# Performance work log

Hardware: AMD Instinct MI355X
Metric: run time of the kernel (lower is better)

The kernel has to match this reference:

```python
import jax, jax.numpy as jnp
import numpy as np

DN = ('NHWC', 'HWIO', 'NHWC')

def _conv(x, k):
    return jax.lax.conv_general_dilated(x, k, (1, 1), 'SAME', dimension_numbers=DN)

def _hard_sigmoid(x):
    # Keras ConvLSTM2D default recurrent_activation
    return jnp.clip(0.2 * x + 0.5, 0.0, 1.0)

def _convlstm2d(x, K, R, b):
    # x: [B,T,H,W,Cin]; K: [kh,kw,Cin,4F]; R: [kh,kw,F,4F]; b: [4F]
    B, T, H, W, C = x.shape
    F = R.shape[2]
    # precompute input-to-gate convs for all timesteps at once
    xz = _conv(x.reshape(B * T, H, W, C), K).reshape(B, T, H, W, 4 * F) + b
    xz = jnp.swapaxes(xz, 0, 1)  # [T,B,H,W,4F]
    h0 = jnp.zeros((B, H, W, F), x.dtype)
    c0 = jnp.zeros((B, H, W, F), x.dtype)

    def step(carry, xt):
        h, c = carry
        z = xt + _conv(h, R)  # [B,H,W,4F]
        zi, zf, zg, zo = jnp.split(z, 4, axis=-1)  # keras gate order i,f,c,o
        c_new = _hard_sigmoid(zf) * c + _hard_sigmoid(zi) * jnp.tanh(zg)
        h_new = _hard_sigmoid(zo) * jnp.tanh(c_new)
        return (h_new, c_new), h_new

    _, hs = jax.lax.scan(step, (h0, c0), xz)  # hs: [T,B,H,W,F]
    return jnp.swapaxes(hs, 0, 1)  # [B,T,H,W,F]

def setup_inputs() -> dict:
    key = jax.random.key(0)
    ks = jax.random.split(key, 6)
    B, T, H, W, Cin, F = 4, 8, 64, 64, 32, 64
    s = 0.05  # keep gates out of saturation
    return {
        'x': jax.random.normal(ks[0], (B, T, H, W, Cin), dtype=jnp.float32),
        'K1': jax.random.normal(ks[1], (5, 5, Cin, 4 * F), dtype=jnp.float32) * s,
        'R1': jax.random.normal(ks[2], (5, 5, F, 4 * F), dtype=jnp.float32) * s,
        'b1': jnp.zeros((4 * F,), dtype=jnp.float32),
        'K2': jax.random.normal(ks[3], (3, 3, F, 4 * F), dtype=jnp.float32) * s,
        'R2': jax.random.normal(ks[4], (3, 3, F, 4 * F), dtype=jnp.float32) * s,
        'b2': jnp.zeros((4 * F,), dtype=jnp.float32),
    }

def reference(x, K1, R1, b1, K2, R2, b2):
    # RecurrentConvBlock with normalization=None, dropout_rate=0:
    # Y = relu(ConvLSTM2D_1(X)); Y = relu(ConvLSTM2D_2(Y))
    y = jax.nn.relu(_convlstm2d(x, K1, R1, b1))
    y = jax.nn.relu(_convlstm2d(y, K2, R2, b2))
    return y
```

## Files before the change

### kernel.cpp

```cpp
#include <hip/hip_runtime.h>

typedef __attribute__((ext_vector_type(4))) float f32x4;
typedef __attribute__((ext_vector_type(8))) short s16x8;

#define MFMA16(a, b, c) __builtin_amdgcn_mfma_f32_16x16x32_bf16((a), (b), (c), 0, 0, 0)

__device__ __forceinline__ float hsig(float x) {
    return fminf(fmaxf(0.2f * x + 0.5f, 0.0f), 1.0f);
}

__device__ __forceinline__ unsigned short bf16rne(float v) {
    unsigned u = __float_as_uint(v);
    u += 0x7FFFu + ((u >> 16) & 1u);
    return (unsigned short)(u >> 16);
}

template<int KHW, int CX, int NS>
__global__ __launch_bounds__(256)
void prep_w(const float* __restrict__ Kw, const float* __restrict__ Rw,
            unsigned short* __restrict__ Bw)
{
    int gid = blockIdx.x * 256 + threadIdx.x;
    if (gid >= NS * 1024) return;
    int lane  = gid & 63;
    int nfrag = (gid >> 6) & 15;
    int ks    = gid >> 10;
    int n   = nfrag * 16 + (lane & 15);
    int src = (n & 3) * 64 + (n >> 2);
    int kl  = (lane >> 4) * 8;
    constexpr int KX = KHW * CX;
    s16x8 vh;
#pragma unroll
    for (int j = 0; j < 8; ++j) {
        int kg = ks * 32 + kl + j;
        float w = (kg < KX) ? Kw[(long)kg * 256 + src]
                            : Rw[(long)(kg - KX) * 256 + src];
        vh[j] = (short)bf16rne(w);
    }
    unsigned short* o = Bw + (long)ks * 8192 + nfrag * 512 + lane * 8;
    *(s16x8*)o = vh;
}

template<int C, int TS, int PAD, int CST>
__device__ __forceinline__ void stage_bf16(const float* __restrict__ gp,
                                           unsigned short* __restrict__ dst,
                                           int ty0, int tx0, int tid)
{
    constexpr int CH = C / 8;
    constexpr int NP = TS * TS;
    for (int i = tid; i < NP * CH; i += 512) {
        int ch = i % CH;
        int p  = i / CH;
        int py = p / TS, px = p % TS;
        int iy = ty0 + py - PAD, ix = tx0 + px - PAD;
        s16x8 vb;
        if (iy >= 0 && iy < 64 && ix >= 0 && ix < 64) {
            const float* s = gp + ((long)(iy * 64 + ix)) * C + ch * 8;
            f32x4 a = *(const f32x4*)s;
            f32x4 b = *(const f32x4*)(s + 4);
#pragma unroll
            for (int j = 0; j < 4; ++j) {
                vb[j]     = (short)bf16rne(a[j]);
                vb[4 + j] = (short)bf16rne(b[j]);
            }
        } else {
#pragma unroll
            for (int j = 0; j < 8; ++j) vb[j] = 0;
        }
        *(s16x8*)(dst + ch * CST + p * 8) = vb;
    }
}

template<int KW, int CX, int TS, int NS, int XS>
__device__ __forceinline__ void lstm_body(
    unsigned short* __restrict__ smem,
    float* __restrict__ hplane,
    const float* __restrict__ xin, long xbstride,
    const float* __restrict__ hin,
    const unsigned short* __restrict__ Bg,
    const float* __restrict__ bias,
    float* __restrict__ c_buf,
    float* __restrict__ h_out,
    float* __restrict__ y_out, long ybstride,
    int b)
{
    constexpr int PAD = KW / 2;
    constexpr int NP  = TS * TS;
    constexpr int CHX = CX / 8;
    constexpr int CST = NP * 8;
    constexpr int XPLANE = CHX * CST;

    unsigned short* sx = smem;
    unsigned short* sh = sx + XPLANE;

    const int tid  = threadIdx.x;
    const int lane = tid & 63, wid = tid >> 6;
    const int ty0 = blockIdx.y * 8, tx0 = blockIdx.x * 8;

    const unsigned short* bq = Bg + (2 * wid) * 512 + lane * 8;

    stage_bf16<CX, TS, PAD, CST>(xin + (long)b * xbstride, sx, ty0, tx0, tid);
    stage_bf16<64, TS, PAD, CST>(hin + (long)b * 4096 * 64, sh, ty0, tx0, tid);
    __syncthreads();

    f32x4 acc[2][4];
#pragma unroll
    for (int cf = 0; cf < 2; ++cf)
#pragma unroll
        for (int pf = 0; pf < 4; ++pf)
#pragma unroll
            for (int q = 0; q < 4; ++q) acc[cf][pf][q] = 0.0f;

    const int pb  = lane & 15;
    const int kq  = (lane >> 4) * CST;
    const int av0 = (((pb      >> 3) * TS) + (pb      & 7)) * 8 + kq;
    const int av1 = ((((pb+16) >> 3) * TS) + ((pb+16) & 7)) * 8 + kq;
    const int av2 = ((((pb+32) >> 3) * TS) + ((pb+32) & 7)) * 8 + kq;
    const int av3 = ((((pb+48) >> 3) * TS) + ((pb+48) & 7)) * 8 + kq;

#define KSTEP(PX, SO)                                                     \
    {                                                                     \
        s16x8 W0 = *(const s16x8*)(bq);                                   \
        s16x8 W1 = *(const s16x8*)(bq + 512);                             \
        s16x8 X0 = *(const s16x8*)((PX) + (SO) + av0);                    \
        s16x8 X1 = *(const s16x8*)((PX) + (SO) + av1);                    \
        s16x8 X2 = *(const s16x8*)((PX) + (SO) + av2);                    \
        s16x8 X3 = *(const s16x8*)((PX) + (SO) + av3);                    \
        acc[0][0] = MFMA16(W0, X0, acc[0][0]);                            \
        acc[1][0] = MFMA16(W1, X0, acc[1][0]);                            \
        acc[0][1] = MFMA16(W0, X1, acc[0][1]);                            \
        acc[1][1] = MFMA16(W1, X1, acc[1][1]);                            \
        acc[0][2] = MFMA16(W0, X2, acc[0][2]);                            \
        acc[1][2] = MFMA16(W1, X2, acc[1][2]);                            \
        acc[0][3] = MFMA16(W0, X3, acc[0][3]);                            \
        acc[1][3] = MFMA16(W1, X3, acc[1][3]);                            \
        bq += 8192;                                                       \
    }

    if (CX == 32) {
#pragma unroll 1
        for (int kh = 0; kh < KW; ++kh) {
#pragma unroll
            for (int kw = 0; kw < KW; ++kw) {
                KSTEP(sx, (kh * TS + kw) * 8);
            }
        }
    } else {
#pragma unroll 1
        for (int kh = 0; kh < KW; ++kh) {
#pragma unroll
            for (int kw = 0; kw < KW; ++kw) {
#pragma unroll
                for (int c2 = 0; c2 < 2; ++c2) {
                    KSTEP(sx, c2 * 4 * CST + (kh * TS + kw) * 8);
                }
            }
        }
    }
#pragma unroll 1
    for (int kh = 0; kh < KW; ++kh) {
#pragma unroll
        for (int kw = 0; kw < KW; ++kw) {
#pragma unroll
            for (int c2 = 0; c2 < 2; ++c2) {
                KSTEP(sh, c2 * 4 * CST + (kh * TS + kw) * 8);
            }
        }
    }
#undef KSTEP

    const int pxb  = lane & 15;
    const int fq   = lane >> 4;
    const int tile = blockIdx.y * 8 + blockIdx.x;
    const long cb0 = (((long)b * 64 + tile) * 8) * 512 + tid;
#pragma unroll
    for (int cf = 0; cf < 2; ++cf) {
        const int f = wid * 8 + cf * 4 + fq;
        const float bi  = bias[f];
        const float bfr = bias[64 + f];
        const float bg  = bias[128 + f];
        const float bo  = bias[192 + f];
#pragma unroll
        for (int pf = 0; pf < 4; ++pf) {
            int p   = pf * 16 + pxb;
            long oc = cb0 + (long)(cf * 4 + pf) * 512;
            float zi = acc[cf][pf][0] + bi;
            float zf = acc[cf][pf][1] + bfr;
            float zg = acc[cf][pf][2] + bg;
            float zo = acc[cf][pf][3] + bo;
            float cv = c_buf[oc];
            float cn = hsig(zf) * cv + hsig(zi) * tanhf(zg);
            c_buf[oc] = cn;
            hplane[p * 65 + f] = hsig(zo) * tanhf(cn);
        }
    }
    __syncthreads();

    const int f = tid & 63;
#pragma unroll
    for (int j = 0; j < 8; ++j) {
        int p  = (tid >> 6) + j * 8;
        int yy = ty0 + (p >> 3), xx = tx0 + (p & 7);
        int gp = yy * 64 + xx;
        float hn = hplane[p * 65 + f];
        long o = ((long)(b * 64 + yy) * 64 + xx) * 64 + f;
        h_out[o] = hn;
        y_out[(long)b * ybstride + (long)gp * 64 + f] = fmaxf(hn, 0.0f);
    }
}

__global__ __launch_bounds__(512, 2)
void lstm_fused(
    const float* __restrict__ x1, const float* __restrict__ h1in,
    const unsigned short* __restrict__ B1g, const float* __restrict__ bias1,
    float* __restrict__ c1, float* __restrict__ h1out, float* __restrict__ y1out,
    const float* __restrict__ x2, const float* __restrict__ h2in,
    const unsigned short* __restrict__ B2g, const float* __restrict__ bias2,
    float* __restrict__ c2, float* __restrict__ h2out, float* __restrict__ y2out,
    int mode)
{
    __shared__ __align__(16) unsigned short smem[13824];
    __shared__ __align__(16) float hplane[64 * 65];
    const int z = blockIdx.z;
    const int b = z & 3;
    const bool doL2 = (mode == 1) || (z >= 4);
    if (!doL2) {
        lstm_body<5, 32, 12, 75, 25>(smem, hplane, x1, (long)8 * 4096 * 32, h1in,
                                     B1g, bias1, c1, h1out,
                                     y1out, (long)8 * 4096 * 64, b);
    } else {
        lstm_body<3, 64, 10, 36, 18>(smem, hplane, x2, (long)8 * 4096 * 64, h2in,
                                     B2g, bias2, c2, h2out,
                                     y2out, (long)8 * 4096 * 64, b);
    }
}

extern "C" void kernel_launch(void* const* d_in, const int* in_sizes, int n_in,
                              void* d_out, int out_size, void* d_ws, size_t ws_size,
                              hipStream_t stream)
{
    const float* x  = (const float*)d_in[0];
    const float* K1 = (const float*)d_in[1];
    const float* R1 = (const float*)d_in[2];
    const float* b1 = (const float*)d_in[3];
    const float* K2 = (const float*)d_in[4];
    const float* R2 = (const float*)d_in[5];
    const float* b2 = (const float*)d_in[6];
    float* out = (float*)d_out;

    const long HW   = 4096;
    const long SZ_S = HW * 64 * 4;
    const long SZ_Y = SZ_S * 8;

    float* ws  = (float*)d_ws;
    float* y1  = ws;
    float* h1a = y1 + SZ_Y;
    float* h1b = h1a + SZ_S;
    float* h2a = h1b + SZ_S;
    float* h2b = h2a + SZ_S;
    float* c1  = h2b + SZ_S;
    float* c2  = c1 + SZ_S;
    unsigned short* B1 = (unsigned short*)(c2 + SZ_S);
    unsigned short* B2 = B1 + (long)75 * 8192;

    prep_w<25, 32, 75><<<300, 256, 0, stream>>>(K1, R1, B1);
    prep_w<9,  64, 36><<<144, 256, 0, stream>>>(K2, R2, B2);

    hipMemsetAsync(h1a, 0, (size_t)SZ_S * sizeof(float), stream);
    hipMemsetAsync(c1,  0, (size_t)SZ_S * sizeof(float), stream);
    hipMemsetAsync(h2a, 0, (size_t)SZ_S * sizeof(float), stream);
    hipMemsetAsync(c2,  0, (size_t)SZ_S * sizeof(float), stream);

    float* hp1 = h1a; float* hn1 = h1b;
    float* hp2 = h2a; float* hn2 = h2b;

    for (int t = 0; t <= 8; ++t) {
        const int mode = (t == 0) ? 0 : (t == 8) ? 1 : 2;
        const int t1  = (t <= 7) ? t : 7;
        const int tm1 = (t >= 1) ? t - 1 : 0;
        dim3 grid(8, 8, mode == 2 ? 8 : 4);
        lstm_fused<<<grid, 512, 0, stream>>>(
            x  + (long)t1 * HW * 32,  hp1, B1, b1, c1, hn1,
            y1 + (long)t1 * HW * 64,
            y1 + (long)tm1 * HW * 64, hp2, B2, b2, c2, hn2,
            out + (long)tm1 * HW * 64,
            mode);
        if (mode != 1) { float* tmp = hp1; hp1 = hn1; hn1 = tmp; }
        if (mode != 0) { float* tmp = hp2; hp2 = hn2; hn2 = tmp; }
    }
}
```

Measured before the change: 354.3 us.

## Fully unroll K loop with register double-buffered operands and drop state memsets

Replaces the partially unrolled KSTEP loops with a fully unrolled schedule built from a constexpr offset table. Weight and activation fragments for the next k-step are prefetched into double-buffered registers while the current MFMAs run, and MFMA issue priority is raised with s_setprio. The four hipMemsetAsync calls for the initial h/c state are removed: a zero-init flag instead skips loading h and c on the first timestep of each layer. Full unrolling of 75 steps raises code size and register pressure, which may hurt occupancy at 2 blocks per CU.

```diff
diff --git a/kernel.cpp b/kernel.cpp
--- a/kernel.cpp
+++ b/kernel.cpp
@@ -44,7 +44,7 @@
 template<int C, int TS, int PAD, int CST>
 __device__ __forceinline__ void stage_bf16(const float* __restrict__ gp,
                                            unsigned short* __restrict__ dst,
-                                           int ty0, int tx0, int tid)
+                                           int ty0, int tx0, int tid, bool zero)
 {
     constexpr int CH = C / 8;
     constexpr int NP = TS * TS;
@@ -54,7 +54,7 @@
         int py = p / TS, px = p % TS;
         int iy = ty0 + py - PAD, ix = tx0 + px - PAD;
         s16x8 vb;
-        if (iy >= 0 && iy < 64 && ix >= 0 && ix < 64) {
+        if (!zero && iy >= 0 && iy < 64 && ix >= 0 && ix < 64) {
             const float* s = gp + ((long)(iy * 64 + ix)) * C + ch * 8;
             f32x4 a = *(const f32x4*)s;
             f32x4 b = *(const f32x4*)(s + 4);
@@ -69,6 +69,34 @@
         }
         *(s16x8*)(dst + ch * CST + p * 8) = vb;
     }
+}
+
+template<int KW, int CX, int TS, int NS, int XS>
+struct KSched { int so[NS]; int hp[NS]; };
+
+template<int KW, int CX, int TS, int NS, int XS>
+constexpr KSched<KW, CX, TS, NS, XS> make_sched() {
+    KSched<KW, CX, TS, NS, XS> s{};
+    constexpr int CST = TS * TS * 8;
+    int i = 0;
+    if (CX == 32) {
+        for (int kh = 0; kh < KW; ++kh)
+            for (int kw = 0; kw < KW; ++kw) {
+                s.so[i] = (kh * TS + kw) * 8; s.hp[i] = 0; ++i;
+            }
+    } else {
+        for (int kh = 0; kh < KW; ++kh)
+            for (int kw = 0; kw < KW; ++kw)
+                for (int c2 = 0; c2 < 2; ++c2) {
+                    s.so[i] = c2 * 4 * CST + (kh * TS + kw) * 8; s.hp[i] = 0; ++i;
+                }
+    }
+    for (int kh = 0; kh < KW; ++kh)
+        for (int kw = 0; kw < KW; ++kw)
+            for (int c2 = 0; c2 < 2; ++c2) {
+                s.so[i] = c2 * 4 * CST + (kh * TS + kw) * 8; s.hp[i] = 1; ++i;
+            }
+    return s;
 }
 
 template<int KW, int CX, int TS, int NS, int XS>
@@ -82,13 +110,14 @@
     float* __restrict__ c_buf,
     float* __restrict__ h_out,
     float* __restrict__ y_out, long ybstride,
-    int b)
+    int b, bool zi)
 {
     constexpr int PAD = KW / 2;
     constexpr int NP  = TS * TS;
     constexpr int CHX = CX / 8;
     constexpr int CST = NP * 8;
     constexpr int XPLANE = CHX * CST;
+    constexpr auto SC = make_sched<KW, CX, TS, NS, XS>();
 
     unsigned short* sx = smem;
     unsigned short* sh = sx + XPLANE;
@@ -99,8 +128,12 @@
 
     const unsigned short* bq = Bg + (2 * wid) * 512 + lane * 8;
 
-    stage_bf16<CX, TS, PAD, CST>(xin + (long)b * xbstride, sx, ty0, tx0, tid);
-    stage_bf16<64, TS, PAD, CST>(hin + (long)b * 4096 * 64, sh, ty0, tx0, tid);
+    s16x8 Wb[2][2];
+    Wb[0][0] = *(const s16x8*)(bq);
+    Wb[0][1] = *(const s16x8*)(bq + 512);
+
+    stage_bf16<CX, TS, PAD, CST>(xin + (long)b * xbstride, sx, ty0, tx0, tid, false);
+    stage_bf16<64, TS, PAD, CST>(hin + (long)b * 4096 * 64, sh, ty0, tx0, tid, zi);
     __syncthreads();
 
     f32x4 acc[2][4];
@@ -118,56 +151,38 @@
     const int av2 = ((((pb+32) >> 3) * TS) + ((pb+32) & 7)) * 8 + kq;
     const int av3 = ((((pb+48) >> 3) * TS) + ((pb+48) & 7)) * 8 + kq;
 
-#define KSTEP(PX, SO)                                                     \
-    {                                                                     \
-        s16x8 W0 = *(const s16x8*)(bq);                                   \
-        s16x8 W1 = *(const s16x8*)(bq + 512);                             \
-        s16x8 X0 = *(const s16x8*)((PX) + (SO) + av0);                    \
-        s16x8 X1 = *(const s16x8*)((PX) + (SO) + av1);                    \
-        s16x8 X2 = *(const s16x8*)((PX) + (SO) + av2);                    \
-        s16x8 X3 = *(const s16x8*)((PX) + (SO) + av3);                    \
-        acc[0][0] = MFMA16(W0, X0, acc[0][0]);                            \
-        acc[1][0] = MFMA16(W1, X0, acc[1][0]);                            \
-        acc[0][1] = MFMA16(W0, X1, acc[0][1]);                            \
-        acc[1][1] = MFMA16(W1, X1, acc[1][1]);                            \
-        acc[0][2] = MFMA16(W0, X2, acc[0][2]);                            \
-        acc[1][2] = MFMA16(W1, X2, acc[1][2]);                            \
-        acc[0][3] = MFMA16(W0, X3, acc[0][3]);                            \
-        acc[1][3] = MFMA16(W1, X3, acc[1][3]);                            \
-        bq += 8192;                                                       \
-    }
-
-    if (CX == 32) {
-#pragma unroll 1
-        for (int kh = 0; kh < KW; ++kh) {
-#pragma unroll
-            for (int kw = 0; kw < KW; ++kw) {
-                KSTEP(sx, (kh * TS + kw) * 8);
-            }
+    s16x8 Xb[2][4];
+    {
+        const unsigned short* pp = SC.hp[0] ? sh : sx;
+        Xb[0][0] = *(const s16x8*)(pp + SC.so[0] + av0);
+        Xb[0][1] = *(const s16x8*)(pp + SC.so[0] + av1);
+        Xb[0][2] = *(const s16x8*)(pp + SC.so[0] + av2);
+        Xb[0][3] = *(const s16x8*)(pp + SC.so[0] + av3);
+    }
+
+#pragma unroll
+    for (int ks = 0; ks < NS; ++ks) {
+        if (ks + 1 < NS) {
+            Wb[(ks + 1) & 1][0] = *(const s16x8*)(bq + 8192);
+            Wb[(ks + 1) & 1][1] = *(const s16x8*)(bq + 8192 + 512);
+            const unsigned short* pp = SC.hp[ks + 1] ? sh : sx;
+            Xb[(ks + 1) & 1][0] = *(const s16x8*)(pp + SC.so[ks + 1] + av0);
+            Xb[(ks + 1) & 1][1] = *(const s16x8*)(pp + SC.so[ks + 1] + av1);
+            Xb[(ks + 1) & 1][2] = *(const s16x8*)(pp + SC.so[ks + 1] + av2);
+            Xb[(ks + 1) & 1][3] = *(const s16x8*)(pp + SC.so[ks + 1] + av3);
         }
-    } else {
-#pragma unroll 1
-        for (int kh = 0; kh < KW; ++kh) {
-#pragma unroll
-            for (int kw = 0; kw < KW; ++kw) {
-#pragma unroll
-                for (int c2 = 0; c2 < 2; ++c2) {
-                    KSTEP(sx, c2 * 4 * CST + (kh * TS + kw) * 8);
-                }
-            }
-        }
-    }
-#pragma unroll 1
-    for (int kh = 0; kh < KW; ++kh) {
-#pragma unroll
-        for (int kw = 0; kw < KW; ++kw) {
-#pragma unroll
-            for (int c2 = 0; c2 < 2; ++c2) {
-                KSTEP(sh, c2 * 4 * CST + (kh * TS + kw) * 8);
-            }
-        }
-    }
-#undef KSTEP
+        __builtin_amdgcn_s_setprio(1);
+        acc[0][0] = MFMA16(Wb[ks & 1][0], Xb[ks & 1][0], acc[0][0]);
+        acc[1][0] = MFMA16(Wb[ks & 1][1], Xb[ks & 1][0], acc[1][0]);
+        acc[0][1] = MFMA16(Wb[ks & 1][0], Xb[ks & 1][1], acc[0][1]);
+        acc[1][1] = MFMA16(Wb[ks & 1][1], Xb[ks & 1][1], acc[1][1]);
+        acc[0][2] = MFMA16(Wb[ks & 1][0], Xb[ks & 1][2], acc[0][2]);
+        acc[1][2] = MFMA16(Wb[ks & 1][1], Xb[ks & 1][2], acc[1][2]);
+        acc[0][3] = MFMA16(Wb[ks & 1][0], Xb[ks & 1][3], acc[0][3]);
+        acc[1][3] = MFMA16(Wb[ks & 1][1], Xb[ks & 1][3], acc[1][3]);
+        __builtin_amdgcn_s_setprio(0);
+        bq += 8192;
+    }
 
     const int pxb  = lane & 15;
     const int fq   = lane >> 4;
@@ -184,12 +199,12 @@
         for (int pf = 0; pf < 4; ++pf) {
             int p   = pf * 16 + pxb;
             long oc = cb0 + (long)(cf * 4 + pf) * 512;
-            float zi = acc[cf][pf][0] + bi;
-            float zf = acc[cf][pf][1] + bfr;
-            float zg = acc[cf][pf][2] + bg;
-            float zo = acc[cf][pf][3] + bo;
-            float cv = c_buf[oc];
-            float cn = hsig(zf) * cv + hsig(zi) * tanhf(zg);
+            float zif = acc[cf][pf][0] + bi;
+            float zf  = acc[cf][pf][1] + bfr;
+            float zg  = acc[cf][pf][2] + bg;
+            float zo  = acc[cf][pf][3] + bo;
+            float cv = zi ? 0.0f : c_buf[oc];
+            float cn = hsig(zf) * cv + hsig(zif) * tanhf(zg);
             c_buf[oc] = cn;
             hplane[p * 65 + f] = hsig(zo) * tanhf(cn);
         }
@@ -217,7 +232,7 @@
     const float* __restrict__ x2, const float* __restrict__ h2in,
     const unsigned short* __restrict__ B2g, const float* __restrict__ bias2,
     float* __restrict__ c2, float* __restrict__ h2out, float* __restrict__ y2out,
-    int mode)
+    int mode, int zf)
 {
     __shared__ __align__(16) unsigned short smem[13824];
     __shared__ __align__(16) float hplane[64 * 65];
@@ -227,11 +242,11 @@
     if (!doL2) {
         lstm_body<5, 32, 12, 75, 25>(smem, hplane, x1, (long)8 * 4096 * 32, h1in,
                                      B1g, bias1, c1, h1out,
-                                     y1out, (long)8 * 4096 * 64, b);
+                                     y1out, (long)8 * 4096 * 64, b, (zf & 1) != 0);
     } else {
         lstm_body<3, 64, 10, 36, 18>(smem, hplane, x2, (long)8 * 4096 * 64, h2in,
                                      B2g, bias2, c2, h2out,
-                                     y2out, (long)8 * 4096 * 64, b);
+                                     y2out, (long)8 * 4096 * 64, b, (zf & 2) != 0);
     }
 }
 
@@ -266,16 +281,12 @@
     prep_w<25, 32, 75><<<300, 256, 0, stream>>>(K1, R1, B1);
     prep_w<9,  64, 36><<<144, 256, 0, stream>>>(K2, R2, B2);
 
-    hipMemsetAsync(h1a, 0, (size_t)SZ_S * sizeof(float), stream);
-    hipMemsetAsync(c1,  0, (size_t)SZ_S * sizeof(float), stream);
-    hipMemsetAsync(h2a, 0, (size_t)SZ_S * sizeof(float), stream);
-    hipMemsetAsync(c2,  0, (size_t)SZ_S * sizeof(float), stream);
-
     float* hp1 = h1a; float* hn1 = h1b;
     float* hp2 = h2a; float* hn2 = h2b;
 
     for (int t = 0; t <= 8; ++t) {
         const int mode = (t == 0) ? 0 : (t == 8) ? 1 : 2;
+        const int zf   = (t == 0 ? 1 : 0) | (t == 1 ? 2 : 0);
         const int t1  = (t <= 7) ? t : 7;
         const int tm1 = (t >= 1) ? t - 1 : 0;
         dim3 grid(8, 8, mode == 2 ? 8 : 4);
@@ -284,7 +295,7 @@
             y1 + (long)t1 * HW * 64,
             y1 + (long)tm1 * HW * 64, hp2, B2, b2, c2, hn2,
             out + (long)tm1 * HW * 64,
-            mode);
+            mode, zf);
         if (mode != 1) { float* tmp = hp1; hp1 = hn1; hn1 = tmp; }
         if (mode != 0) { float* tmp = hp2; hp2 = hn2; hn2 = tmp; }
     }
```

After: 289.3 us. 18.3% less time.
